# Optimization experiments

Hardware: AMD Instinct MI355X
Metric: run time of the kernel (lower is better)

Reference implementation:

```python
import jax, jax.numpy as jnp
import numpy as np

N_NODES = 100000
N_EDGES = 3200000
F_IN, F_HID, F_OUT = 36, 8, 2
NEG_SLOPE = 0.2


def gat_layer(x, src, dst, W, a_src, a_dst, b, num_nodes):
    # Linear transform: [N, F'] 
    h = x @ W
    # Per-node attention logits (heads=1)
    alpha_s = h @ a_src  # [N]
    alpha_d = h @ a_dst  # [N]
    # Edge-wise score: leaky_relu(a_src . h_j + a_dst . h_i) for edge j->i
    e = jax.nn.leaky_relu(alpha_s[src] + alpha_d[dst], negative_slope=NEG_SLOPE)  # [E]
    # Segment softmax over incoming edges of each dst node
    m = jax.ops.segment_max(e, dst, num_segments=num_nodes)  # [N]
    ee = jnp.exp(e - m[dst])
    denom = jax.ops.segment_sum(ee, dst, num_segments=num_nodes)  # [N]
    alpha = ee / denom[dst]  # [E]
    # Scatter-aggregate messages
    out = jax.ops.segment_sum(alpha[:, None] * h[src], dst, num_segments=num_nodes)
    return out + b


def setup_inputs() -> dict:
    key = jax.random.key(0)
    ks = jax.random.split(key, 10)
    x = jax.random.normal(ks[0], (N_NODES, F_IN), dtype=jnp.float32)
    edge_index = jax.random.randint(ks[1], (2, N_EDGES), 0, N_NODES, dtype=jnp.int64)
    s1 = 1.0 / np.sqrt(F_IN)
    s2 = 1.0 / np.sqrt(F_HID)
    W1 = jax.random.uniform(ks[2], (F_IN, F_HID), jnp.float32, -s1, s1)
    a_src1 = jax.random.uniform(ks[3], (F_HID,), jnp.float32, -s2, s2)
    a_dst1 = jax.random.uniform(ks[4], (F_HID,), jnp.float32, -s2, s2)
    b1 = jnp.zeros((F_HID,), jnp.float32)
    W2 = jax.random.uniform(ks[5], (F_HID, F_OUT), jnp.float32, -s2, s2)
    so = 1.0 / np.sqrt(F_OUT)
    a_src2 = jax.random.uniform(ks[6], (F_OUT,), jnp.float32, -so, so)
    a_dst2 = jax.random.uniform(ks[7], (F_OUT,), jnp.float32, -so, so)
    b2 = jnp.zeros((F_OUT,), jnp.float32)
    return {"x": x, "edge_index": edge_index, "W1": W1, "a_src1": a_src1,
            "a_dst1": a_dst1, "b1": b1, "W2": W2, "a_src2": a_src2,
            "a_dst2": a_dst2, "b2": b2}


def reference(x, edge_index, W1, a_src1, a_dst1, b1, W2, a_src2, a_dst2, b2):
    src, dst = edge_index[0], edge_index[1]
    n = x.shape[0]
    h = jax.nn.relu(gat_layer(x, src, dst, W1, a_src1, a_dst1, b1, n))
    # dropout is identity in eval mode
    out = gat_layer(h, src, dst, W2, a_src2, a_dst2, b2, n)
    return jax.nn.log_softmax(out, axis=1)
```

## Files before the change

### kernel.cpp

```cpp
#include <hip/hip_runtime.h>
#include <hip/hip_bf16.h>

#define N_NODES 100000
#define N_EDGES 3200000
#define F_IN 36
#define F_HID 8
#define F_OUT 2
#define NEG_SLOPE 0.2f

#define GSHIFT 7
#define GNPB 128
#define GNBUCK 782
#define CAP 4608
#define NB_PART 256
#define CHUNK 12500
#define BP 1024
#define BPG 512

__device__ __forceinline__ int detect_is64(const void* eidx, int* s_flag) {
    if (threadIdx.x < 64) {
        const unsigned int* p = (const unsigned int*)eidx;
        unsigned int v1 = p[2 * threadIdx.x + 1];
        unsigned int v2 = p[2 * (threadIdx.x + 64) + 1];
        unsigned long long m = __ballot(v1 != 0u || v2 != 0u);
        if (threadIdx.x == 0) *s_flag = (m == 0ull) ? 1 : 0;
    }
    __syncthreads();
    return *s_flag;
}

__global__ void partition1_k(const void* __restrict__ eidx, int* __restrict__ gcnt,
                             int* __restrict__ partP) {
    __shared__ int h[GNBUCK];
    __shared__ int s_flag;
    int t = threadIdx.x;
    for (int i = t; i < GNBUCK; i += BP) h[i] = 0;
    int f = detect_is64(eidx, &s_flag);
    int beg = blockIdx.x * CHUNK;
    int end = beg + CHUNK; if (end > N_EDGES) end = N_EDGES;
    if (f) {
        const long long* p = (const long long*)eidx;
        for (int i = beg + t; i < end; i += BP) atomicAdd(&h[(int)p[N_EDGES + i] >> GSHIFT], 1);
    } else {
        const int* p = (const int*)eidx;
        for (int i = beg + t; i < end; i += BP) atomicAdd(&h[p[N_EDGES + i] >> GSHIFT], 1);
    }
    __syncthreads();
    for (int i = t; i < GNBUCK; i += BP) {
        int c = h[i];
        h[i] = c ? atomicAdd(&gcnt[i], c) : 0;
    }
    __syncthreads();
    if (f) {
        const long long* p = (const long long*)eidx;
        for (int i = beg + t; i < end; i += BP) {
            int s = (int)p[i];
            int d = (int)p[N_EDGES + i];
            int b = d >> GSHIFT;
            int pos = atomicAdd(&h[b], 1);
            if (pos < CAP) partP[b * CAP + pos] = (s << GSHIFT) | (d & (GNPB - 1));
        }
    } else {
        const int* p = (const int*)eidx;
        for (int i = beg + t; i < end; i += BP) {
            int s = p[i];
            int d = p[N_EDGES + i];
            int b = d >> GSHIFT;
            int pos = atomicAdd(&h[b], 1);
            if (pos < CAP) partP[b * CAP + pos] = (s << GSHIFT) | (d & (GNPB - 1));
        }
    }
}

__global__ void node1_k(const float* __restrict__ x, const float* __restrict__ W1,
                        const float* __restrict__ aw_s, const float* __restrict__ aw_d,
                        float* __restrict__ h1, float* __restrict__ as1, float* __restrict__ ad1,
                        int n_nodes) {
    int n = blockIdx.x * blockDim.x + threadIdx.x;
    if (n >= n_nodes) return;
    float acc[F_HID];
#pragma unroll
    for (int f = 0; f < F_HID; f++) acc[f] = 0.f;
    const float4* xp = (const float4*)(x + (size_t)n * F_IN);
#pragma unroll
    for (int q = 0; q < 9; q++) {
        float4 xv = xp[q];
        const float* w = W1 + q * 4 * F_HID;
#pragma unroll
        for (int f = 0; f < F_HID; f++) {
            acc[f] += xv.x * w[0 * F_HID + f] + xv.y * w[1 * F_HID + f]
                    + xv.z * w[2 * F_HID + f] + xv.w * w[3 * F_HID + f];
        }
    }
    float s = 0.f, d = 0.f;
#pragma unroll
    for (int f = 0; f < F_HID; f++) {
        s += acc[f] * aw_s[f];
        d += acc[f] * aw_d[f];
    }
    float4* hp = (float4*)(h1 + (size_t)n * F_HID);
    hp[0] = make_float4(acc[0], acc[1], acc[2], acc[3]);
    hp[1] = make_float4(acc[4], acc[5], acc[6], acc[7]);
    as1[n] = s;
    ad1[n] = d;
}

__global__ void gatF1_k(const int* __restrict__ gcnt, const int* __restrict__ partP,
                        int* __restrict__ e_srcP, int2* __restrict__ rowinfo,
                        const float* __restrict__ as1, const float* __restrict__ ad1,
                        const float* __restrict__ h1, const float* __restrict__ b1,
                        const float* __restrict__ W2, const float* __restrict__ aw_s2,
                        const float* __restrict__ aw_d2, float4* __restrict__ P2) {
    __shared__ int eL[CAP];
    __shared__ int hist[GNPB];
    __shared__ int nstart[GNPB];
    __shared__ int cursor[GNPB];
    __shared__ int sscan[GNPB];
    __shared__ float adl[GNPB];
    int t = threadIdx.x;
    int c = blockIdx.x;
    int nbase = c << GSHIFT;
    int beg = c * CAP;
    int cnt = gcnt[c]; if (cnt > CAP) cnt = CAP;

    if (t < GNPB) {
        hist[t] = 0;
        adl[t] = (nbase + t < N_NODES) ? ad1[nbase + t] : 0.f;
    }
    __syncthreads();
    for (int j = t; j < cnt; j += BPG)
        atomicAdd(&hist[partP[beg + j] & (GNPB - 1)], 1);
    __syncthreads();
    if (t < GNPB) sscan[t] = hist[t];
    __syncthreads();
    for (int o = 1; o < GNPB; o <<= 1) {
        int u = (t < GNPB && t >= o) ? sscan[t - o] : 0;
        __syncthreads();
        if (t < GNPB) sscan[t] += u;
        __syncthreads();
    }
    if (t < GNPB) {
        int ex = sscan[t] - hist[t];
        nstart[t] = ex;
        cursor[t] = ex;
        int node = nbase + t;
        if (node < N_NODES) rowinfo[node] = make_int2(beg + ex, hist[t]);
    }
    __syncthreads();
    for (int j = t; j < cnt; j += BPG) {
        int pk = partP[beg + j];
        int pos = atomicAdd(&cursor[pk & (GNPB - 1)], 1);
        eL[pos] = pk >> GSHIFT;
    }
    __syncthreads();
    for (int i = t; i < cnt; i += BPG) e_srcP[beg + i] = eL[i];

    int node = t >> 2;
    int lane = t & 3;
    int gnode = nbase + node;
    if (gnode >= N_NODES) return;
    int ns = nstart[node];
    int ne = ns + hist[node];
    float add = adl[node];

    float denom = 0.f;
    float acc[F_HID];
#pragma unroll
    for (int f = 0; f < F_HID; f++) acc[f] = 0.f;
    for (int i = ns + lane; i < ne; i += 4) {
        int s = eL[i];
        float e = as1[s] + add;
        e = e >= 0.f ? e : NEG_SLOPE * e;
        float ee = __expf(e);
        denom += ee;
        const float4* hp = (const float4*)(h1 + (size_t)s * F_HID);
        float4 p0 = hp[0], p1 = hp[1];
        acc[0] += ee * p0.x; acc[1] += ee * p0.y; acc[2] += ee * p0.z; acc[3] += ee * p0.w;
        acc[4] += ee * p1.x; acc[5] += ee * p1.y; acc[6] += ee * p1.z; acc[7] += ee * p1.w;
    }
#pragma unroll
    for (int o = 2; o > 0; o >>= 1) {
        denom += __shfl_xor(denom, o, 4);
#pragma unroll
        for (int f = 0; f < F_HID; f++) acc[f] += __shfl_xor(acc[f], o, 4);
    }
    if (lane == 0) {
        float inv = denom > 0.f ? 1.f / denom : 0.f;
        float o0 = 0.f, o1 = 0.f;
#pragma unroll
        for (int f = 0; f < F_HID; f++) {
            float v = acc[f] * inv + b1[f];
            v = v > 0.f ? v : 0.f;
            o0 += v * W2[f * F_OUT + 0];
            o1 += v * W2[f * F_OUT + 1];
        }
        float as2v = o0 * aw_s2[0] + o1 * aw_s2[1];
        float ad2v = o0 * aw_d2[0] + o1 * aw_d2[1];
        P2[gnode] = make_float4(as2v, o0, o1, ad2v);
    }
}

__global__ void gat2_k(const int2* __restrict__ rowinfo, const int* __restrict__ e_srcP,
                       const float4* __restrict__ P2, const float* __restrict__ b2,
                       float* __restrict__ out, int n_nodes) {
    int gid = blockIdx.x * 16 + (threadIdx.x >> 4);
    int lane = threadIdx.x & 15;
    if (gid >= n_nodes) return;
    int2 ri = rowinfo[gid];
    float add = P2[gid].w;

    float denom = 0.f, a0 = 0.f, a1 = 0.f;
    int jend = ri.x + ri.y;
    for (int j = ri.x + lane; j < jend; j += 16) {
        int s = e_srcP[j];
        float4 q = P2[s];
        float e = q.x + add;
        e = e >= 0.f ? e : NEG_SLOPE * e;
        float ee = __expf(e);
        denom += ee;
        a0 += ee * q.y;
        a1 += ee * q.z;
    }
#pragma unroll
    for (int o = 8; o > 0; o >>= 1) {
        denom += __shfl_xor(denom, o, 16);
        a0 += __shfl_xor(a0, o, 16);
        a1 += __shfl_xor(a1, o, 16);
    }

    if (lane == 0) {
        float inv = denom > 0.f ? 1.f / denom : 0.f;
        float o0 = a0 * inv + b2[0];
        float o1 = a1 * inv + b2[1];
        float M = fmaxf(o0, o1);
        float l = M + logf(__expf(o0 - M) + __expf(o1 - M));
        ((float2*)out)[gid] = make_float2(o0 - l, o1 - l);
    }
}

extern "C" void kernel_launch(void* const* d_in, const int* in_sizes, int n_in,
                              void* d_out, int out_size, void* d_ws, size_t ws_size,
                              hipStream_t stream) {
    const float* x      = (const float*)d_in[0];
    const void*  eidx   = d_in[1];
    const float* W1     = (const float*)d_in[2];
    const float* a_src1 = (const float*)d_in[3];
    const float* a_dst1 = (const float*)d_in[4];
    const float* b1     = (const float*)d_in[5];
    const float* W2     = (const float*)d_in[6];
    const float* a_src2 = (const float*)d_in[7];
    const float* a_dst2 = (const float*)d_in[8];
    const float* b2     = (const float*)d_in[9];
    float* out = (float*)d_out;

    const size_t N = N_NODES;
    const size_t PADDED = (size_t)GNBUCK * CAP;

    int* wsi = (int*)d_ws;
    float* wsf = (float*)d_ws;
    size_t o = 0;
    int* partP    = wsi + o;      o += PADDED;
    int* e_srcP   = wsi + o;      o += PADDED;
    int* gcnt     = wsi + o;      o += 800;
    int2* rowinfo = (int2*)(wsi + o); o += 2 * N;
    float* as1    = wsf + o;      o += N;
    float* ad1    = wsf + o;      o += N;
    float* h1     = wsf + o;      o += 8 * N;
    float4* P2    = (float4*)(wsf + o); o += 4 * N;

    const int B = 256;
    const int gridN = (int)((N + B - 1) / B);
    const int gridG = (int)(N / 16);

    hipMemsetAsync(gcnt, 0, 800 * sizeof(int), stream);

    partition1_k<<<NB_PART, BP, 0, stream>>>(eidx, gcnt, partP);
    node1_k<<<gridN, B, 0, stream>>>(x, W1, a_src1, a_dst1, h1, as1, ad1, (int)N);
    gatF1_k<<<GNBUCK, BPG, 0, stream>>>(gcnt, partP, e_srcP, rowinfo, as1, ad1, h1, b1,
                                        W2, a_src2, a_dst2, P2);
    gat2_k<<<gridG, B, 0, stream>>>(rowinfo, e_srcP, P2, b2, out, (int)N);
}
```

Baseline: 185.0 us.

## Split edge partition into coarse 1024-node pass then fine 128-node pass

Replaces the single-pass scatter of edges into 782 fine destination buckets with a two-level partition: first into 98 coarse buckets of 1024 nodes, then a second kernel splits each coarse bucket into 8 fine buckets. The intent is to make the first scatter's writes more coalesced, since 98 buckets receive longer contiguous runs than 782. The cost is an extra kernel and another full read and write of the edge array. The e_srcP buffer now aliases the coarse partition buffer to save workspace, which is safe only because part2 finishes before gatF1 writes to it.

```diff
diff --git a/kernel.cpp b/kernel.cpp
--- a/kernel.cpp
+++ b/kernel.cpp
@@ -8,13 +8,17 @@
 #define F_OUT 2
 #define NEG_SLOPE 0.2f
 
+#define SHIFT_C 10
+#define NCB 98
+#define CAPC 36000
 #define GSHIFT 7
 #define GNPB 128
 #define GNBUCK 782
-#define CAP 4608
+#define CAPF 4480
 #define NB_PART 256
 #define CHUNK 12500
 #define BP 1024
+#define BP2 512
 #define BPG 512
 
 __device__ __forceinline__ int detect_is64(const void* eidx, int* s_flag) {
@@ -29,26 +33,26 @@
     return *s_flag;
 }
 
-__global__ void partition1_k(const void* __restrict__ eidx, int* __restrict__ gcnt,
-                             int* __restrict__ partP) {
-    __shared__ int h[GNBUCK];
+__global__ void part1_k(const void* __restrict__ eidx, int* __restrict__ gcnt_c,
+                        int* __restrict__ partC) {
+    __shared__ int h[NCB];
     __shared__ int s_flag;
     int t = threadIdx.x;
-    for (int i = t; i < GNBUCK; i += BP) h[i] = 0;
+    if (t < NCB) h[t] = 0;
     int f = detect_is64(eidx, &s_flag);
     int beg = blockIdx.x * CHUNK;
     int end = beg + CHUNK; if (end > N_EDGES) end = N_EDGES;
     if (f) {
         const long long* p = (const long long*)eidx;
-        for (int i = beg + t; i < end; i += BP) atomicAdd(&h[(int)p[N_EDGES + i] >> GSHIFT], 1);
+        for (int i = beg + t; i < end; i += BP) atomicAdd(&h[(int)p[N_EDGES + i] >> SHIFT_C], 1);
     } else {
         const int* p = (const int*)eidx;
-        for (int i = beg + t; i < end; i += BP) atomicAdd(&h[p[N_EDGES + i] >> GSHIFT], 1);
-    }
-    __syncthreads();
-    for (int i = t; i < GNBUCK; i += BP) {
-        int c = h[i];
-        h[i] = c ? atomicAdd(&gcnt[i], c) : 0;
+        for (int i = beg + t; i < end; i += BP) atomicAdd(&h[p[N_EDGES + i] >> SHIFT_C], 1);
+    }
+    __syncthreads();
+    if (t < NCB) {
+        int c = h[t];
+        h[t] = c ? atomicAdd(&gcnt_c[t], c) : 0;
     }
     __syncthreads();
     if (f) {
@@ -56,19 +60,51 @@
         for (int i = beg + t; i < end; i += BP) {
             int s = (int)p[i];
             int d = (int)p[N_EDGES + i];
-            int b = d >> GSHIFT;
+            int b = d >> SHIFT_C;
             int pos = atomicAdd(&h[b], 1);
-            if (pos < CAP) partP[b * CAP + pos] = (s << GSHIFT) | (d & (GNPB - 1));
+            if (pos < CAPC) partC[b * CAPC + pos] = (s << SHIFT_C) | (d & 1023);
         }
     } else {
         const int* p = (const int*)eidx;
         for (int i = beg + t; i < end; i += BP) {
             int s = p[i];
             int d = p[N_EDGES + i];
-            int b = d >> GSHIFT;
+            int b = d >> SHIFT_C;
             int pos = atomicAdd(&h[b], 1);
-            if (pos < CAP) partP[b * CAP + pos] = (s << GSHIFT) | (d & (GNPB - 1));
+            if (pos < CAPC) partC[b * CAPC + pos] = (s << SHIFT_C) | (d & 1023);
         }
+    }
+}
+
+__global__ void part2_k(const int* __restrict__ gcnt_c, const int* __restrict__ partC,
+                        int* __restrict__ gcnt_f, int* __restrict__ fineP) {
+    __shared__ int h8[8];
+    __shared__ int cur8[8];
+    int t = threadIdx.x;
+    int cb = blockIdx.x >> 3;
+    int k = blockIdx.x & 7;
+    int cntc = gcnt_c[cb]; if (cntc > CAPC) cntc = CAPC;
+    int sbeg = (int)((long long)k * cntc / 8);
+    int send = (int)((long long)(k + 1) * cntc / 8);
+    const int* cp = partC + (size_t)cb * CAPC;
+
+    if (t < 8) h8[t] = 0;
+    __syncthreads();
+    for (int j = sbeg + t; j < send; j += BP2)
+        atomicAdd(&h8[(cp[j] >> GSHIFT) & 7], 1);
+    __syncthreads();
+    if (t < 8) {
+        int c = h8[t];
+        cur8[t] = c ? atomicAdd(&gcnt_f[cb * 8 + t], c) : 0;
+    }
+    __syncthreads();
+    for (int j = sbeg + t; j < send; j += BP2) {
+        int pk = cp[j];
+        int fidx = (pk >> GSHIFT) & 7;
+        int pos = atomicAdd(&cur8[fidx], 1);
+        if (pos < CAPF)
+            fineP[(size_t)(cb * 8 + fidx) * CAPF + pos] =
+                ((pk >> SHIFT_C) << GSHIFT) | (pk & (GNPB - 1));
     }
 }
 
@@ -105,13 +141,13 @@
     ad1[n] = d;
 }
 
-__global__ void gatF1_k(const int* __restrict__ gcnt, const int* __restrict__ partP,
+__global__ void gatF1_k(const int* __restrict__ gcnt_f, const int* __restrict__ fineP,
                         int* __restrict__ e_srcP, int2* __restrict__ rowinfo,
                         const float* __restrict__ as1, const float* __restrict__ ad1,
                         const float* __restrict__ h1, const float* __restrict__ b1,
                         const float* __restrict__ W2, const float* __restrict__ aw_s2,
                         const float* __restrict__ aw_d2, float4* __restrict__ P2) {
-    __shared__ int eL[CAP];
+    __shared__ int eL[CAPF];
     __shared__ int hist[GNPB];
     __shared__ int nstart[GNPB];
     __shared__ int cursor[GNPB];
@@ -120,8 +156,8 @@
     int t = threadIdx.x;
     int c = blockIdx.x;
     int nbase = c << GSHIFT;
-    int beg = c * CAP;
-    int cnt = gcnt[c]; if (cnt > CAP) cnt = CAP;
+    size_t beg = (size_t)c * CAPF;
+    int cnt = gcnt_f[c]; if (cnt > CAPF) cnt = CAPF;
 
     if (t < GNPB) {
         hist[t] = 0;
@@ -129,7 +165,7 @@
     }
     __syncthreads();
     for (int j = t; j < cnt; j += BPG)
-        atomicAdd(&hist[partP[beg + j] & (GNPB - 1)], 1);
+        atomicAdd(&hist[fineP[beg + j] & (GNPB - 1)], 1);
     __syncthreads();
     if (t < GNPB) sscan[t] = hist[t];
     __syncthreads();
@@ -144,11 +180,11 @@
         nstart[t] = ex;
         cursor[t] = ex;
         int node = nbase + t;
-        if (node < N_NODES) rowinfo[node] = make_int2(beg + ex, hist[t]);
+        if (node < N_NODES) rowinfo[node] = make_int2((int)beg + ex, hist[t]);
     }
     __syncthreads();
     for (int j = t; j < cnt; j += BPG) {
-        int pk = partP[beg + j];
+        int pk = fineP[beg + j];
         int pos = atomicAdd(&cursor[pk & (GNPB - 1)], 1);
         eL[pos] = pk >> GSHIFT;
     }
@@ -254,14 +290,17 @@
     float* out = (float*)d_out;
 
     const size_t N = N_NODES;
-    const size_t PADDED = (size_t)GNBUCK * CAP;
+    const size_t SZC = (size_t)NCB * CAPC;
+    const size_t SZF = (size_t)784 * CAPF;
 
     int* wsi = (int*)d_ws;
     float* wsf = (float*)d_ws;
     size_t o = 0;
-    int* partP    = wsi + o;      o += PADDED;
-    int* e_srcP   = wsi + o;      o += PADDED;
-    int* gcnt     = wsi + o;      o += 800;
+    int* partC    = wsi + o;      o += SZC;
+    int* e_srcP   = partC;
+    int* fineP    = wsi + o;      o += SZF;
+    int* gcnt_c   = wsi + o;      o += 128;
+    int* gcnt_f   = wsi + o;      o += 800;
     int2* rowinfo = (int2*)(wsi + o); o += 2 * N;
     float* as1    = wsf + o;      o += N;
     float* ad1    = wsf + o;      o += N;
@@ -272,11 +311,12 @@
     const int gridN = (int)((N + B - 1) / B);
     const int gridG = (int)(N / 16);
 
-    hipMemsetAsync(gcnt, 0, 800 * sizeof(int), stream);
-
-    partition1_k<<<NB_PART, BP, 0, stream>>>(eidx, gcnt, partP);
+    hipMemsetAsync(gcnt_c, 0, (128 + 800) * sizeof(int), stream);
+
+    part1_k<<<NB_PART, BP, 0, stream>>>(eidx, gcnt_c, partC);
+    part2_k<<<NCB * 8, BP2, 0, stream>>>(gcnt_c, partC, gcnt_f, fineP);
     node1_k<<<gridN, B, 0, stream>>>(x, W1, a_src1, a_dst1, h1, as1, ad1, (int)N);
-    gatF1_k<<<GNBUCK, BPG, 0, stream>>>(gcnt, partP, e_srcP, rowinfo, as1, ad1, h1, b1,
+    gatF1_k<<<GNBUCK, BPG, 0, stream>>>(gcnt_f, fineP, e_srcP, rowinfo, as1, ad1, h1, b1,
                                         W2, a_src2, a_dst2, P2);
     gat2_k<<<gridG, B, 0, stream>>>(rowinfo, e_srcP, P2, b2, out, (int)N);
 }
```

Result: slower. 191.7 us (+3.6%).
